# Kernel optimization log

Hardware: AMD Instinct MI355X
Metric: run time of the kernel (lower is better)

The kernel has to match this reference:

```python
import jax, jax.numpy as jnp
import numpy as np

EPS = 1e-5
FIXED = 6  # attention_dim


def _layernorm(x, g, b):
    mu = x.mean(-1, keepdims=True)
    var = ((x - mu) ** 2).mean(-1, keepdims=True)
    return (x - mu) * jax.lax.rsqrt(var + EPS) * g + b


def _mha(x, Wqkv, bqkv, Wo, bo, num_heads):
    # x: [B,S,D]; torch nn.MultiheadAttention (batch_first), attn weights averaged over heads
    B, S, D = x.shape
    hd = D // num_heads
    qkv = x @ Wqkv.T + bqkv                      # [B,S,3D]
    q, k, v = jnp.split(qkv, 3, axis=-1)
    sh = lambda t: t.reshape(B, S, num_heads, hd).transpose(0, 2, 1, 3)  # [B,H,S,hd]
    q, k, v = sh(q), sh(k), sh(v)
    scores = jnp.einsum('bhqd,bhkd->bhqk', q, k) / np.sqrt(hd).astype(np.float32)
    attn = jax.nn.softmax(scores, axis=-1)
    out = jnp.einsum('bhqk,bhkd->bhqd', attn, v).transpose(0, 2, 1, 3).reshape(B, S, D)
    return out @ Wo.T + bo, attn.mean(axis=1)    # [B,S,D], [B,S,S]


def _gcn(x, edge_index, W, b):
    # PyG GCNConv: add self-loops, symmetric normalization, aggregate into dst
    N = x.shape[0]
    loop = jnp.arange(N, dtype=edge_index.dtype)
    src = jnp.concatenate([edge_index[0], loop])
    dst = jnp.concatenate([edge_index[1], loop])
    deg = jax.ops.segment_sum(jnp.ones(src.shape[0], x.dtype), dst, num_segments=N)
    dinv = jax.lax.rsqrt(jnp.maximum(deg, 1.0))  # deg >= 1 with self-loops
    norm = dinv[src] * dinv[dst]                 # [E+N]
    h = x @ W.T                                  # [N,D]
    msg = h[src] * norm[:, None]
    return jax.ops.segment_sum(msg, dst, num_segments=N) + b


def setup_inputs() -> dict:
    key = jax.random.key(0)
    ks = jax.random.split(key, 24)
    D = 768
    N, E, U, K, B, S = 100000, 1600000, 1024, 32, 8, 126
    w = lambda k, shp: jax.random.normal(k, shp, jnp.float32) * 0.02
    return {
        'user_text': jax.random.normal(ks[0], (B, S, D), jnp.float32),
        'all_user_feature': jax.random.normal(ks[1], (N, D), jnp.float32),
        'user_neighbor_index': jax.random.randint(ks[2], (U, K), 0, N),
        'edge_index': jax.random.randint(ks[3], (2, E), 0, N),
        # LModel (text transformer block) params
        'Wqkv_l': w(ks[4], (3 * D, D)), 'bqkv_l': jnp.zeros((3 * D,), jnp.float32),
        'Wo_l': w(ks[5], (D, D)), 'bo_l': jnp.zeros((D,), jnp.float32),
        'ln1_g': jnp.ones((D,), jnp.float32), 'ln1_b': jnp.zeros((D,), jnp.float32),
        'ln2_g': jnp.ones((D,), jnp.float32), 'ln2_b': jnp.zeros((D,), jnp.float32),
        'W1': w(ks[6], (D, D)), 'b1': jnp.zeros((D,), jnp.float32),
        'W2': w(ks[7], (D, D)), 'b2': jnp.zeros((D,), jnp.float32),
        # GCNConv params
        'Wg': w(ks[8], (D, D)), 'bg': jnp.zeros((D,), jnp.float32),
        # MultiAttn (per-neighborhood attention) params
        'Wqkv_m': w(ks[9], (3 * D, D)), 'bqkv_m': jnp.zeros((3 * D,), jnp.float32),
        'Wo_m': w(ks[10], (D, D)), 'bo_m': jnp.zeros((D,), jnp.float32),
    }


def reference(user_text, all_user_feature, user_neighbor_index, edge_index,
              Wqkv_l, bqkv_l, Wo_l, bo_l, ln1_g, ln1_b, ln2_g, ln2_b,
              W1, b1, W2, b2, Wg, bg, Wqkv_m, bqkv_m, Wo_m, bo_m):
    # --- LModel: pre-norm transformer block (dropout = eval identity) ---
    sa, attn_w = _mha(_layernorm(user_text, ln1_g, ln1_b), Wqkv_l, bqkv_l, Wo_l, bo_l, 4)
    text = user_text + sa
    h = jax.nn.leaky_relu(_layernorm(text, ln2_g, ln2_b) @ W1.T + b1)  # LeakyReLU(0.01)
    text = text + (h @ W2.T + b2)

    # --- GCN over the user graph (NeighborSampler sizes=[-1] == full 1-hop) ---
    feats = _gcn(all_user_feature, edge_index, Wg, bg)

    # --- MultiAttn: self-attention within each neighborhood, write back center ---
    nb = feats[user_neighbor_index]                       # [U,K,D] gather
    nb_out, _ = _mha(nb, Wqkv_m, bqkv_m, Wo_m, bo_m, 4)   # batched over U
    feats = feats.at[user_neighbor_index[:, 0]].set(nb_out[:, 0, :])

    # --- FixedPooling: adaptive avg-pool attention map [B,S,S] -> [B,6,6] ---
    B, S, _ = attn_w.shape
    p = S // FIXED
    attention_graph = attn_w.reshape(B, FIXED, p, FIXED, p).mean(axis=(2, 4))
    return text, feats, attention_graph
```

## Files before the change

### kernel.cpp

```cpp
#include <hip/hip_runtime.h>
#include <hip/hip_bf16.h>
#include <stdint.h>

typedef __attribute__((ext_vector_type(8))) short short8;
typedef __attribute__((ext_vector_type(4))) float f32x4;
typedef __attribute__((ext_vector_type(2))) unsigned int u32x2;

__device__ __forceinline__ float bf2f(uint32_t u16) {
    union { uint32_t i; float f; } v; v.i = u16 << 16; return v.f;
}
__device__ __forceinline__ uint16_t f2bf(float f) {
    union { float f; uint32_t i; } v; v.f = f;
    uint32_t r = v.i + 0x7fffu + ((v.i >> 16) & 1u);
    return (uint16_t)(r >> 16);
}
__device__ __forceinline__ short8 cvt8(const float* p) {
    const float2* f2 = (const float2*)p;
    union { __hip_bfloat162 h[4]; short8 s; } c;
    c.h[0] = __float22bfloat162_rn(f2[0]);
    c.h[1] = __float22bfloat162_rn(f2[1]);
    c.h[2] = __float22bfloat162_rn(f2[2]);
    c.h[3] = __float22bfloat162_rn(f2[3]);
    return c.s;
}

__global__ void code_write_f32(float* __restrict__ out, int n, float codef)
{
    int i = blockIdx.x * 256 + threadIdx.x;
    if (i < n) out[i] = codef;
}

__global__ __launch_bounds__(256) void gemm_bt(
    const float* __restrict__ A, const float* __restrict__ W,
    const float* __restrict__ bias, void* __restrict__ Cv,
    const float* __restrict__ R, const int* __restrict__ rowmap, int rstride,
    int M, int N, int act, int cbf)
{
    const int K = 768;
    int numN = N >> 7;
    int numM = (M + 127) >> 7;
    int lid = blockIdx.x;
    int x = lid & 7, j = lid >> 3;
    int bm_local = j / numN, bn = j - bm_local * numN;
    int q = numM >> 3, rr = numM & 7;
    int cnt = q + (x < rr ? 1 : 0);
    if (bm_local >= cnt) return;
    int bm = x * q + min(x, rr) + bm_local;

    __shared__ __attribute__((aligned(16))) uint16_t As[4096];
    __shared__ __attribute__((aligned(16))) uint16_t Ws[4096];
    int tid = threadIdx.x, wv = tid >> 6, ln = tid & 63;
    int wm = wv >> 1, wn = wv & 1;

    const f32x4 zero4 = {0.f, 0.f, 0.f, 0.f};
    f32x4 acc[4][4];
#pragma unroll
    for (int i = 0; i < 4; ++i)
#pragma unroll
        for (int jj = 0; jj < 4; ++jj) acc[i][jj] = zero4;

    int r0 = tid >> 2, cb = tid & 3;
    int c8 = cb * 8;
    int r1 = r0 + 64;
    int ar0 = min(bm * 128 + r0, M - 1);
    int ar1 = min(bm * 128 + r1, M - 1);
    if (rowmap) { ar0 = rowmap[(size_t)ar0 * rstride]; ar1 = rowmap[(size_t)ar1 * rstride]; }
    int br0 = bn * 128 + r0, br1 = bn * 128 + r1;
    const float* Af0 = A + (size_t)ar0 * K + c8;
    const float* Af1 = A + (size_t)ar1 * K + c8;
    const float* Wf0 = W + (size_t)br0 * K + c8;
    const float* Wf1 = W + (size_t)br1 * K + c8;
    const int sw  = (cb ^ (r0 & 3)) * 8;
    const int s0 = r0 * 32 + sw;
    const int s1 = 2048 + r0 * 32 + sw;
    const int lr = ln & 15, kg = ln >> 4;
    const int kgsw = (kg ^ (lr & 3)) * 8;

    for (int k0 = 0; k0 < K; k0 += 32) {
        short8 a0 = cvt8(Af0 + k0);
        short8 a1 = cvt8(Af1 + k0);
        short8 w0 = cvt8(Wf0 + k0);
        short8 w1 = cvt8(Wf1 + k0);
        __syncthreads();
        *(short8*)&As[s0] = a0;
        *(short8*)&As[s1] = a1;
        *(short8*)&Ws[s0] = w0;
        *(short8*)&Ws[s1] = w1;
        __syncthreads();
        short8 afr[4], bfr[4];
#pragma unroll
        for (int mi = 0; mi < 4; ++mi)
            afr[mi] = *(const short8*)&As[(wm * 64 + mi * 16 + lr) * 32 + kgsw];
#pragma unroll
        for (int nj = 0; nj < 4; ++nj)
            bfr[nj] = *(const short8*)&Ws[(wn * 64 + nj * 16 + lr) * 32 + kgsw];
#pragma unroll
        for (int mi = 0; mi < 4; ++mi)
#pragma unroll
            for (int nj = 0; nj < 4; ++nj)
                acc[mi][nj] = __builtin_amdgcn_mfma_f32_16x16x32_bf16(
                    afr[mi], bfr[nj], acc[mi][nj], 0, 0, 0);
    }

#pragma unroll
    for (int mi = 0; mi < 4; ++mi) {
        int growb = bm * 128 + wm * 64 + mi * 16 + kg * 4;
#pragma unroll
        for (int nj = 0; nj < 4; ++nj) {
            int gcol = bn * 128 + wn * 64 + nj * 16 + lr;
            float bs = bias ? bias[gcol] : 0.f;
#pragma unroll
            for (int qq = 0; qq < 4; ++qq) {
                int grow = growb + qq;
                if (grow < M) {
                    float val = acc[mi][nj][qq] + bs;
                    if (R) val += R[(size_t)grow * N + gcol];
                    if (act == 1) val = (val > 0.f) ? val : 0.01f * val;
                    size_t idx = (size_t)grow * N + gcol;
                    if (cbf) ((uint16_t*)Cv)[idx] = f2bf(val);
                    else     ((float*)Cv)[idx]    = val;
                }
            }
        }
    }
}

__global__ __launch_bounds__(256) void ln_kernel(
    const float* __restrict__ x, const float* __restrict__ g,
    const float* __restrict__ bb, float* __restrict__ y)
{
    int row = blockIdx.x, tid = threadIdx.x;
    const float* xr = x + (size_t)row * 768;
    float v0 = xr[tid], v1 = xr[tid + 256], v2 = xr[tid + 512];
    float s = v0 + v1 + v2;
    __shared__ float red[4];
#pragma unroll
    for (int mk = 32; mk >= 1; mk >>= 1) s += __shfl_xor(s, mk);
    int wv = tid >> 6, ln = tid & 63;
    if (ln == 0) red[wv] = s;
    __syncthreads();
    float mu = (red[0] + red[1] + red[2] + red[3]) * (1.f / 768.f);
    float d0 = v0 - mu, d1 = v1 - mu, d2 = v2 - mu;
    float ss = d0 * d0 + d1 * d1 + d2 * d2;
#pragma unroll
    for (int mk = 32; mk >= 1; mk >>= 1) ss += __shfl_xor(ss, mk);
    __syncthreads();
    if (ln == 0) red[wv] = ss;
    __syncthreads();
    float var = (red[0] + red[1] + red[2] + red[3]) * (1.f / 768.f);
    float inv = 1.0f / sqrtf(var + 1e-5f);
    float* yr = y + (size_t)row * 768;
    yr[tid]       = d0 * inv * g[tid]       + bb[tid];
    yr[tid + 256] = d1 * inv * g[tid + 256] + bb[tid + 256];
    yr[tid + 512] = d2 * inv * g[tid + 512] + bb[tid + 512];
}

__global__ __launch_bounds__(256) void nattn(
    const float* __restrict__ qkv, float* __restrict__ attnout,
    float* __restrict__ pooled)
{
    int b = blockIdx.x / 126, i = blockIdx.x % 126;
    int tid = threadIdx.x;
    __shared__ float P[4][128];
    __shared__ float poolloc[6];
    if (tid < 6) poolloc[tid] = 0.f;
    const size_t base = (size_t)b * 126 * 2304;
    const float scale = 0.0721687836f;

    for (int p = tid; p < 504; p += 256) {
        int h = p / 126, j = p - h * 126;
        const float* qr = qkv + base + (size_t)i * 2304 + h * 192;
        const float* kr = qkv + base + (size_t)j * 2304 + 768 + h * 192;
        float a = 0.f;
#pragma unroll 8
        for (int d = 0; d < 192; ++d) a += qr[d] * kr[d];
        P[h][j] = a * scale;
    }
    __syncthreads();

    {
        int w = tid >> 6, ln = tid & 63;
        bool v1 = (ln + 64) < 126;
        float s0 = P[w][ln];
        float s1 = v1 ? P[w][ln + 64] : -1e30f;
        float m = fmaxf(s0, s1);
#pragma unroll
        for (int mk = 32; mk >= 1; mk >>= 1) m = fmaxf(m, __shfl_xor(m, mk));
        float e0 = __expf(s0 - m);
        float e1 = v1 ? __expf(s1 - m) : 0.f;
        float z = e0 + e1;
#pragma unroll
        for (int mk = 32; mk >= 1; mk >>= 1) z += __shfl_xor(z, mk);
        float rz = 1.f / z;
        P[w][ln] = e0 * rz;
        if (v1) P[w][ln + 64] = e1 * rz;
    }
    __syncthreads();

    if (tid < 126) {
        float s4 = P[0][tid] + P[1][tid] + P[2][tid] + P[3][tid];
        atomicAdd(&poolloc[tid / 21], s4);
    }

    float o[3];
#pragma unroll
    for (int r = 0; r < 3; ++r) {
        int od = tid + r * 256;
        int h = od / 192;
        float a = 0.f;
        for (int j = 0; j < 126; ++j)
            a += P[h][j] * qkv[base + (size_t)j * 2304 + 1536 + od];
        o[r] = a;
    }
    float* orow = attnout + (size_t)(b * 126 + i) * 768;
#pragma unroll
    for (int r = 0; r < 3; ++r) orow[tid + r * 256] = o[r];

    __syncthreads();
    if (tid < 6)
        atomicAdd(&pooled[b * 36 + (i / 21) * 6 + tid], poolloc[tid]);
}

__global__ void pool_fin_kernel(const float* __restrict__ pooled, float* __restrict__ outp)
{
    int i = blockIdx.x * 36 + threadIdx.x;
    outp[i] = pooled[i] * (1.0f / 1764.0f);
}

__global__ void deg_fill_kernel(const int* __restrict__ ei, int E,
                                int* __restrict__ cnt, int* __restrict__ bucket)
{
    int e = blockIdx.x * 256 + threadIdx.x;
    if (e < E) {
        int s = ei[e], d = ei[E + e];
        int p = atomicAdd(&cnt[d], 1);
        if (p < 64) bucket[(size_t)d * 64 + p] = s;
    }
}
__global__ void dinv_kernel(const int* __restrict__ cnt, float* __restrict__ ds, int N)
{
    int i = blockIdx.x * 256 + threadIdx.x;
    if (i < N) ds[i] = 1.0f / sqrtf((float)cnt[i] + 1.0f);
}

__global__ __launch_bounds__(192) void gcn_agg(
    const uint16_t* __restrict__ h, const int* __restrict__ bucket,
    const int* __restrict__ cnt, const float* __restrict__ dsc,
    const float* __restrict__ bg, float* __restrict__ feats)
{
    int v = blockIdx.x;
    int tid = threadIdx.x;
    __shared__ int nbs[64];
    int nb = min(cnt[v], 64);
    if (tid < nb)
        nbs[tid] = __builtin_nontemporal_load(&bucket[(size_t)v * 64 + tid]);
    __syncthreads();
    float sv = dsc[v];
    u32x2 w = ((const u32x2*)(h + (size_t)v * 768))[tid];
    float a0 = bf2f(w.x & 0xffffu) * sv;
    float a1 = bf2f(w.x >> 16)     * sv;
    float a2 = bf2f(w.y & 0xffffu) * sv;
    float a3 = bf2f(w.y >> 16)     * sv;
    for (int e = 0; e < nb; ++e) {
        int s = nbs[e];
        u32x2 u = ((const u32x2*)(h + (size_t)s * 768))[tid];
        float ss = dsc[s];
        a0 += bf2f(u.x & 0xffffu) * ss;
        a1 += bf2f(u.x >> 16)     * ss;
        a2 += bf2f(u.y & 0xffffu) * ss;
        a3 += bf2f(u.y >> 16)     * ss;
    }
    f32x4 bgv = ((const f32x4*)bg)[tid];
    f32x4 o;
    o.x = a0 * sv + bgv.x;
    o.y = a1 * sv + bgv.y;
    o.z = a2 * sv + bgv.z;
    o.w = a3 * sv + bgv.w;
    __builtin_nontemporal_store(o, &((f32x4*)(feats + (size_t)v * 768))[tid]);
}

__global__ __launch_bounds__(256) void attn_m_kernel(
    const float* __restrict__ kv, const float* __restrict__ qc,
    float* __restrict__ out0)
{
    int u = blockIdx.x;
    int tid = threadIdx.x, h = tid >> 6, ln = tid & 63;
    const float scale = 0.0721687836f;
    float s = -1e30f;
    {
        int j = (ln < 32) ? ln : 0;
        const float* qr = qc + (size_t)u * 768 + h * 192;
        const float* kr = kv + ((size_t)u * 32 + j) * 1536 + h * 192;
        float a = 0.f;
#pragma unroll 8
        for (int d = 0; d < 192; ++d) a += qr[d] * kr[d];
        if (ln < 32) s = a * scale;
    }
    float m = s;
#pragma unroll
    for (int mk = 32; mk >= 1; mk >>= 1) m = fmaxf(m, __shfl_xor(m, mk));
    float e = (ln < 32) ? __expf(s - m) : 0.f;
    float z = e;
#pragma unroll
    for (int mk = 32; mk >= 1; mk >>= 1) z += __shfl_xor(z, mk);
    __shared__ float pbuf[4][32];
    if (ln < 32) pbuf[h][ln] = e / z;
    __syncthreads();
    float a0 = 0.f, a1 = 0.f, a2 = 0.f;
    for (int j = 0; j < 32; ++j) {
        const float* vr = kv + ((size_t)u * 32 + j) * 1536 + 768 + h * 192;
        float p = pbuf[h][j];
        a0 += p * vr[ln]; a1 += p * vr[ln + 64]; a2 += p * vr[ln + 128];
    }
    float* o = out0 + (size_t)u * 768 + h * 192;
    o[ln] = a0; o[ln + 64] = a1; o[ln + 128] = a2;
}

__global__ void winner_kernel(const int* __restrict__ nbidx, int* __restrict__ slot, int U)
{
    int u = blockIdx.x * 256 + threadIdx.x;
    if (u < U) atomicMax(&slot[nbidx[(size_t)u * 32]], u);
}
__global__ __launch_bounds__(256) void scatter_kernel(
    const float* __restrict__ proj, const int* __restrict__ nbidx,
    const int* __restrict__ slot, float* __restrict__ feats)
{
    int u = blockIdx.x;
    int c = nbidx[(size_t)u * 32];
    if (slot[c] != u) return;
    const float* src = proj + (size_t)u * 768;
    float* dst = feats + (size_t)c * 768;
    for (int t = threadIdx.x; t < 768; t += 256) dst[t] = src[t];
}

static inline int gemm_blocks(int M, int N) {
    int numM = (M + 127) >> 7, numN = N >> 7;
    return 8 * ((numM + 7) / 8) * numN;
}

extern "C" void kernel_launch(void* const* d_in, const int* in_sizes, int n_in,
                              void* d_out, int out_size, void* d_ws, size_t ws_size,
                              hipStream_t stream)
{
    const float* user_text = (const float*)d_in[0];
    const float* auf       = (const float*)d_in[1];
    const int*   nbidx     = (const int*)d_in[2];
    const int*   ei        = (const int*)d_in[3];
    const float* Wqkv_l = (const float*)d_in[4];
    const float* bqkv_l = (const float*)d_in[5];
    const float* Wo_l   = (const float*)d_in[6];
    const float* bo_l   = (const float*)d_in[7];
    const float* ln1_g  = (const float*)d_in[8];
    const float* ln1_b  = (const float*)d_in[9];
    const float* ln2_g  = (const float*)d_in[10];
    const float* ln2_b  = (const float*)d_in[11];
    const float* W1 = (const float*)d_in[12];
    const float* b1 = (const float*)d_in[13];
    const float* W2 = (const float*)d_in[14];
    const float* b2 = (const float*)d_in[15];
    const float* Wg = (const float*)d_in[16];
    const float* bg = (const float*)d_in[17];
    const float* Wqkv_m = (const float*)d_in[18];
    const float* bqkv_m = (const float*)d_in[19];
    const float* Wo_m   = (const float*)d_in[20];
    const float* bo_m   = (const float*)d_in[21];

    const int D  = 768;
    const int BS = in_sizes[0] / D;
    const int B  = BS / 126;
    const int N  = in_sizes[1] / D;
    const int U  = in_sizes[2] / 32;
    const int E  = in_sizes[3] / 2;
    const int UK = U * 32;

    float* out_text  = (float*)d_out;
    const int TEXTN = BS * D;
    const int WG_T = (TEXTN + 255) / 256;
    float* out_feats = out_text + (size_t)TEXTN;
    float* out_pool  = out_feats + (size_t)N * D;

    char* ws = (char*)d_ws;
    size_t off = 0;
    auto take = [&](size_t bytes) -> void* {
        void* p = ws + off;
        off += (bytes + 255) & ~(size_t)255;
        return p;
    };
    float* A_h    = (float*)take((size_t)N * D * 4);
    float* qkvl   = (float*)take((size_t)BS * 2304 * 4);
    float* ln1x   = (float*)take((size_t)BS * D * 4);
    float* attnout= (float*)take((size_t)BS * D * 4);
    float* text1  = (float*)take((size_t)BS * D * 4);
    float* ln2x   = (float*)take((size_t)BS * D * 4);
    float* qc     = (float*)take((size_t)U * D * 4);
    float* out0   = (float*)take((size_t)U * D * 4);
    float* projm  = (float*)take((size_t)U * D * 4);
    int*   cnt    = (int*)take((size_t)N * 4);
    float* dsc    = (float*)take((size_t)N * 4);
    int*   slot   = (int*)take((size_t)N * 4);
    int*   bucket = (int*)take((size_t)N * 64 * 4);
    float* pooled = (float*)take((size_t)B * 36 * 4);
    float* hmid   = ln1x;
    uint16_t* hbf = (uint16_t*)A_h;
    float* kv     = A_h;
    size_t required = off;

    if (ws_size < required) {
        code_write_f32<<<WG_T, 256, 0, stream>>>(out_text, TEXTN,
            1.0e6f + (float)(ws_size >> 20) * 1000.0f);
        return;
    }

    hipMemsetAsync(cnt, 0, (size_t)N * 4, stream);
    hipMemsetAsync(slot, 0xFF, (size_t)N * 4, stream);
    hipMemsetAsync(pooled, 0, (size_t)B * 36 * 4, stream);

    deg_fill_kernel<<<(E + 255) / 256, 256, 0, stream>>>(ei, E, cnt, bucket);
    dinv_kernel<<<(N + 255) / 256, 256, 0, stream>>>(cnt, dsc, N);

    ln_kernel<<<BS, 256, 0, stream>>>(user_text, ln1_g, ln1_b, ln1x);
    gemm_bt<<<gemm_blocks(BS, 2304), 256, 0, stream>>>(
        ln1x, Wqkv_l, bqkv_l, qkvl, nullptr, nullptr, 1, BS, 2304, 0, 0);
    nattn<<<BS, 256, 0, stream>>>(qkvl, attnout, pooled);
    gemm_bt<<<gemm_blocks(BS, 768), 256, 0, stream>>>(
        attnout, Wo_l, bo_l, text1, user_text, nullptr, 1, BS, 768, 0, 0);
    ln_kernel<<<BS, 256, 0, stream>>>(text1, ln2_g, ln2_b, ln2x);
    gemm_bt<<<gemm_blocks(BS, 768), 256, 0, stream>>>(
        ln2x, W1, b1, hmid, nullptr, nullptr, 1, BS, 768, 1, 0);
    gemm_bt<<<gemm_blocks(BS, 768), 256, 0, stream>>>(
        hmid, W2, b2, out_text, text1, nullptr, 1, BS, 768, 0, 0);
    pool_fin_kernel<<<B, 36, 0, stream>>>(pooled, out_pool);

    gemm_bt<<<gemm_blocks(N, 768), 256, 0, stream>>>(
        auf, Wg, nullptr, hbf, nullptr, nullptr, 1, N, 768, 0, 1);
    gcn_agg<<<N, 192, 0, stream>>>(hbf, bucket, cnt, dsc, bg, out_feats);

    winner_kernel<<<(U + 255) / 256, 256, 0, stream>>>(nbidx, slot, U);
    gemm_bt<<<gemm_blocks(UK, 1536), 256, 0, stream>>>(
        out_feats, Wqkv_m + (size_t)768 * 768, bqkv_m + 768, kv, nullptr, nbidx, 1, UK, 1536, 0, 0);
    gemm_bt<<<gemm_blocks(U, 768), 256, 0, stream>>>(
        out_feats, Wqkv_m, bqkv_m, qc, nullptr, nbidx, 32, U, 768, 0, 0);
    attn_m_kernel<<<U, 256, 0, stream>>>(kv, qc, out0);
    gemm_bt<<<gemm_blocks(U, 768), 256, 0, stream>>>(
        out0, Wo_m, bo_m, projm, nullptr, nullptr, 1, U, 768, 0, 0);
    scatter_kernel<<<U, 256, 0, stream>>>(projm, nbidx, slot, out_feats);
}
```

Baseline: 1.531 ms.

## Pre-convert weights and node features to bf16; unroll GCN aggregation by two

Adds a grid-stride fp32-to-bf16 conversion kernel. It converts every weight matrix and the large node-feature matrix once per call into workspace buffers. The GEMM then loads bf16 operands directly instead of converting fp32 inside its inner loop, which halves the re-read traffic across N-tiles for the big GCN GEMM. The GCN aggregation loop is also unrolled by two with a second set of accumulators to expose more independent gathers. The tradeoff is extra conversion kernels that read and write the large feature matrix once.

```diff
diff --git a/kernel.cpp b/kernel.cpp
--- a/kernel.cpp
+++ b/kernel.cpp
@@ -30,8 +30,15 @@
     if (i < n) out[i] = codef;
 }
 
+__global__ void f32_to_bf16(const float* __restrict__ in, uint16_t* __restrict__ out, size_t n8)
+{
+    size_t i = (size_t)blockIdx.x * 256 + threadIdx.x;
+    for (; i < n8; i += (size_t)gridDim.x * 256)
+        *(short8*)(out + i * 8) = cvt8(in + i * 8);
+}
+
 __global__ __launch_bounds__(256) void gemm_bt(
-    const float* __restrict__ A, const float* __restrict__ W,
+    const void* __restrict__ Av, int abf, const uint16_t* __restrict__ Wb,
     const float* __restrict__ bias, void* __restrict__ Cv,
     const float* __restrict__ R, const int* __restrict__ rowmap, int rstride,
     int M, int N, int act, int cbf)
@@ -66,10 +73,12 @@
     int ar1 = min(bm * 128 + r1, M - 1);
     if (rowmap) { ar0 = rowmap[(size_t)ar0 * rstride]; ar1 = rowmap[(size_t)ar1 * rstride]; }
     int br0 = bn * 128 + r0, br1 = bn * 128 + r1;
-    const float* Af0 = A + (size_t)ar0 * K + c8;
-    const float* Af1 = A + (size_t)ar1 * K + c8;
-    const float* Wf0 = W + (size_t)br0 * K + c8;
-    const float* Wf1 = W + (size_t)br1 * K + c8;
+    const float*    Af0 = (const float*)Av + (size_t)ar0 * K + c8;
+    const float*    Af1 = (const float*)Av + (size_t)ar1 * K + c8;
+    const uint16_t* Ab0 = (const uint16_t*)Av + (size_t)ar0 * K + c8;
+    const uint16_t* Ab1 = (const uint16_t*)Av + (size_t)ar1 * K + c8;
+    const uint16_t* Wb0 = Wb + (size_t)br0 * K + c8;
+    const uint16_t* Wb1 = Wb + (size_t)br1 * K + c8;
     const int sw  = (cb ^ (r0 & 3)) * 8;
     const int s0 = r0 * 32 + sw;
     const int s1 = 2048 + r0 * 32 + sw;
@@ -77,10 +86,16 @@
     const int kgsw = (kg ^ (lr & 3)) * 8;
 
     for (int k0 = 0; k0 < K; k0 += 32) {
-        short8 a0 = cvt8(Af0 + k0);
-        short8 a1 = cvt8(Af1 + k0);
-        short8 w0 = cvt8(Wf0 + k0);
-        short8 w1 = cvt8(Wf1 + k0);
+        short8 a0, a1;
+        if (abf) {
+            a0 = *(const short8*)(Ab0 + k0);
+            a1 = *(const short8*)(Ab1 + k0);
+        } else {
+            a0 = cvt8(Af0 + k0);
+            a1 = cvt8(Af1 + k0);
+        }
+        short8 w0 = *(const short8*)(Wb0 + k0);
+        short8 w1 = *(const short8*)(Wb1 + k0);
         __syncthreads();
         *(short8*)&As[s0] = a0;
         *(short8*)&As[s1] = a1;
@@ -261,15 +276,32 @@
     float a1 = bf2f(w.x >> 16)     * sv;
     float a2 = bf2f(w.y & 0xffffu) * sv;
     float a3 = bf2f(w.y >> 16)     * sv;
-    for (int e = 0; e < nb; ++e) {
-        int s = nbs[e];
-        u32x2 u = ((const u32x2*)(h + (size_t)s * 768))[tid];
-        float ss = dsc[s];
-        a0 += bf2f(u.x & 0xffffu) * ss;
-        a1 += bf2f(u.x >> 16)     * ss;
-        a2 += bf2f(u.y & 0xffffu) * ss;
-        a3 += bf2f(u.y >> 16)     * ss;
-    }
+    float b0 = 0.f, b1 = 0.f, b2 = 0.f, b3 = 0.f;
+    int e = 0;
+    for (; e + 1 < nb; e += 2) {
+        int sA = nbs[e], sB = nbs[e + 1];
+        u32x2 uA = ((const u32x2*)(h + (size_t)sA * 768))[tid];
+        u32x2 uB = ((const u32x2*)(h + (size_t)sB * 768))[tid];
+        float ssA = dsc[sA], ssB = dsc[sB];
+        a0 += bf2f(uA.x & 0xffffu) * ssA;
+        a1 += bf2f(uA.x >> 16)     * ssA;
+        a2 += bf2f(uA.y & 0xffffu) * ssA;
+        a3 += bf2f(uA.y >> 16)     * ssA;
+        b0 += bf2f(uB.x & 0xffffu) * ssB;
+        b1 += bf2f(uB.x >> 16)     * ssB;
+        b2 += bf2f(uB.y & 0xffffu) * ssB;
+        b3 += bf2f(uB.y >> 16)     * ssB;
+    }
+    if (e < nb) {
+        int sA = nbs[e];
+        u32x2 uA = ((const u32x2*)(h + (size_t)sA * 768))[tid];
+        float ssA = dsc[sA];
+        a0 += bf2f(uA.x & 0xffffu) * ssA;
+        a1 += bf2f(uA.x >> 16)     * ssA;
+        a2 += bf2f(uA.y & 0xffffu) * ssA;
+        a3 += bf2f(uA.y >> 16)     * ssA;
+    }
+    a0 += b0; a1 += b1; a2 += b2; a3 += b3;
     f32x4 bgv = ((const f32x4*)bg)[tid];
     f32x4 o;
     o.x = a0 * sv + bgv.x;
@@ -395,6 +427,13 @@
     float* qc     = (float*)take((size_t)U * D * 4);
     float* out0   = (float*)take((size_t)U * D * 4);
     float* projm  = (float*)take((size_t)U * D * 4);
+    uint16_t* Wqkv_l_b = (uint16_t*)take((size_t)2304 * 768 * 2);
+    uint16_t* Wo_l_b   = (uint16_t*)take((size_t)768 * 768 * 2);
+    uint16_t* W1_b     = (uint16_t*)take((size_t)768 * 768 * 2);
+    uint16_t* W2_b     = (uint16_t*)take((size_t)768 * 768 * 2);
+    uint16_t* Wg_b     = (uint16_t*)take((size_t)768 * 768 * 2);
+    uint16_t* Wqkv_m_b = (uint16_t*)take((size_t)2304 * 768 * 2);
+    uint16_t* Wo_m_b   = (uint16_t*)take((size_t)768 * 768 * 2);
     int*   cnt    = (int*)take((size_t)N * 4);
     float* dsc    = (float*)take((size_t)N * 4);
     int*   slot   = (int*)take((size_t)N * 4);
@@ -402,6 +441,7 @@
     float* pooled = (float*)take((size_t)B * 36 * 4);
     float* hmid   = ln1x;
     uint16_t* hbf = (uint16_t*)A_h;
+    uint16_t* auf_bf = (uint16_t*)A_h + (size_t)N * D;
     float* kv     = A_h;
     size_t required = off;
 
@@ -415,33 +455,42 @@
     hipMemsetAsync(slot, 0xFF, (size_t)N * 4, stream);
     hipMemsetAsync(pooled, 0, (size_t)B * 36 * 4, stream);
 
+    f32_to_bf16<<<2048, 256, 0, stream>>>(auf, auf_bf, (size_t)N * D / 8);
+    f32_to_bf16<<<256, 256, 0, stream>>>(Wqkv_l, Wqkv_l_b, (size_t)2304 * 768 / 8);
+    f32_to_bf16<<<128, 256, 0, stream>>>(Wo_l, Wo_l_b, (size_t)768 * 768 / 8);
+    f32_to_bf16<<<128, 256, 0, stream>>>(W1, W1_b, (size_t)768 * 768 / 8);
+    f32_to_bf16<<<128, 256, 0, stream>>>(W2, W2_b, (size_t)768 * 768 / 8);
+    f32_to_bf16<<<128, 256, 0, stream>>>(Wg, Wg_b, (size_t)768 * 768 / 8);
+    f32_to_bf16<<<256, 256, 0, stream>>>(Wqkv_m, Wqkv_m_b, (size_t)2304 * 768 / 8);
+    f32_to_bf16<<<128, 256, 0, stream>>>(Wo_m, Wo_m_b, (size_t)768 * 768 / 8);
+
     deg_fill_kernel<<<(E + 255) / 256, 256, 0, stream>>>(ei, E, cnt, bucket);
     dinv_kernel<<<(N + 255) / 256, 256, 0, stream>>>(cnt, dsc, N);
 
     ln_kernel<<<BS, 256, 0, stream>>>(user_text, ln1_g, ln1_b, ln1x);
     gemm_bt<<<gemm_blocks(BS, 2304), 256, 0, stream>>>(
-        ln1x, Wqkv_l, bqkv_l, qkvl, nullptr, nullptr, 1, BS, 2304, 0, 0);
+        ln1x, 0, Wqkv_l_b, bqkv_l, qkvl, nullptr, nullptr, 1, BS, 2304, 0, 0);
     nattn<<<BS, 256, 0, stream>>>(qkvl, attnout, pooled);
     gemm_bt<<<gemm_blocks(BS, 768), 256, 0, stream>>>(
-        attnout, Wo_l, bo_l, text1, user_text, nullptr, 1, BS, 768, 0, 0);
+        attnout, 0, Wo_l_b, bo_l, text1, user_text, nullptr, 1, BS, 768, 0, 0);
     ln_kernel<<<BS, 256, 0, stream>>>(text1, ln2_g, ln2_b, ln2x);
     gemm_bt<<<gemm_blocks(BS, 768), 256, 0, stream>>>(
-        ln2x, W1, b1, hmid, nullptr, nullptr, 1, BS, 768, 1, 0);
+        ln2x, 0, W1_b, b1, hmid, nullptr, nullptr, 1, BS, 768, 1, 0);
     gemm_bt<<<gemm_blocks(BS, 768), 256, 0, stream>>>(
-        hmid, W2, b2, out_text, text1, nullptr, 1, BS, 768, 0, 0);
+        hmid, 0, W2_b, b2, out_text, text1, nullptr, 1, BS, 768, 0, 0);
     pool_fin_kernel<<<B, 36, 0, stream>>>(pooled, out_pool);
 
     gemm_bt<<<gemm_blocks(N, 768), 256, 0, stream>>>(
-        auf, Wg, nullptr, hbf, nullptr, nullptr, 1, N, 768, 0, 1);
+        auf_bf, 1, Wg_b, nullptr, hbf, nullptr, nullptr, 1, N, 768, 0, 1);
     gcn_agg<<<N, 192, 0, stream>>>(hbf, bucket, cnt, dsc, bg, out_feats);
 
     winner_kernel<<<(U + 255) / 256, 256, 0, stream>>>(nbidx, slot, U);
     gemm_bt<<<gemm_blocks(UK, 1536), 256, 0, stream>>>(
-        out_feats, Wqkv_m + (size_t)768 * 768, bqkv_m + 768, kv, nullptr, nbidx, 1, UK, 1536, 0, 0);
+        out_feats, 0, Wqkv_m_b + (size_t)768 * 768, bqkv_m + 768, kv, nullptr, nbidx, 1, UK, 1536, 0, 0);
     gemm_bt<<<gemm_blocks(U, 768), 256, 0, stream>>>(
-        out_feats, Wqkv_m, bqkv_m, qc, nullptr, nbidx, 32, U, 768, 0, 0);
+        out_feats, 0, Wqkv_m_b, bqkv_m, qc, nullptr, nbidx, 32, U, 768, 0, 0);
     attn_m_kernel<<<U, 256, 0, stream>>>(kv, qc, out0);
     gemm_bt<<<gemm_blocks(U, 768), 256, 0, stream>>>(
-        out0, Wo_m, bo_m, projm, nullptr, nullptr, 1, U, 768, 0, 0);
+        out0, 0, Wo_m_b, bo_m, projm, nullptr, nullptr, 1, U, 768, 0, 0);
     scatter_kernel<<<U, 256, 0, stream>>>(projm, nbidx, slot, out_feats);
 }
```

New measurement: 1.470 ms. 4.0% less time.
